# Optimization experiments

Hardware: AMD Instinct MI355X
Metric: run time of the kernel (lower is better)

## Reference

```python
import jax, jax.numpy as jnp
import numpy as np

HEADS = 16
HEAD_DIM = 128


def rotate_half(x):
    x1, x2 = x[..., : x.shape[-1] // 2], x[..., x.shape[-1] // 2 :]
    return jnp.concatenate((-x2, x1), axis=-1)


def setup_inputs() -> dict:
    key = jax.random.key(0)
    ks = jax.random.split(key, 8)
    b, s, h = 2, 2048, 2048
    d = HEAD_DIM
    sc = 1.0 / np.sqrt(h)
    x = jax.random.normal(ks[0], (b, s, h), jnp.float32)
    # real RoPE angles for realism
    inv_freq = 1.0 / (10000.0 ** (jnp.arange(0, d, 2, dtype=jnp.float32) / d))
    t = jnp.arange(s, dtype=jnp.float32)
    freqs = jnp.outer(t, inv_freq)  # [s, d/2]
    emb = jnp.concatenate((freqs, freqs), axis=-1)  # [s, d]
    return {
        "x": x,
        "cos": jnp.cos(emb),
        "sin": jnp.sin(emb),
        "wq": jax.random.normal(ks[1], (h, h), jnp.float32) * sc,
        "bq": jnp.zeros((h,), jnp.float32),
        "wk": jax.random.normal(ks[2], (h, h), jnp.float32) * sc,
        "bk": jnp.zeros((h,), jnp.float32),
        "wv": jax.random.normal(ks[3], (h, h), jnp.float32) * sc,
        "bv": jnp.zeros((h,), jnp.float32),
        "wo": jax.random.normal(ks[4], (h, h), jnp.float32) * sc,
    }


def reference(x, cos, sin, wq, bq, wk, bk, wv, bv, wo):
    b, s, hidden = x.shape
    nh, d = HEADS, HEAD_DIM
    # QKV projections (F.linear: x @ W.T + b)
    def split_heads(t):
        return t.reshape(b, s, nh, d).transpose(0, 2, 1, 3)  # [b,h,s,d]
    q = split_heads(x @ wq.T + bq)
    k = split_heads(x @ wk.T + bk)
    v = split_heads(x @ wv.T + bv)
    # RoPE (cos/sin: [s,d] broadcast over [b,h,s,d])
    q = q * cos + rotate_half(q) * sin
    k = k * cos + rotate_half(k) * sin
    # full (non-causal) attention, materializing [b,h,s,s] scores as original
    scale = 1.0 / jnp.sqrt(jnp.asarray(d, x.dtype))
    scores = jnp.einsum("bhqd,bhkd->bhqk", q, k) * scale
    attn = jax.nn.softmax(scores, axis=-1)
    out = jnp.einsum("bhqk,bhkd->bhqd", attn, v)  # [b,h,s,d]
    out = out.transpose(0, 2, 1, 3).reshape(b, s, hidden)
    # o_proj: no bias
    return out @ wo.T
```

## Files before the change

kernel.cpp:

```cpp
#include <hip/hip_runtime.h>

#define B_  2
#define NH  16
#define S_  2048
#define D_  128
#define HID 2048

typedef _Float16 half_t;
typedef _Float16 f16x8 __attribute__((ext_vector_type(8)));
typedef _Float16 f16x4_t __attribute__((ext_vector_type(4)));
typedef float f32x4 __attribute__((ext_vector_type(4)));

__device__ __forceinline__ void glds16(const half_t* g, half_t* l) {
    __builtin_amdgcn_global_load_lds(
        (const __attribute__((address_space(1))) void*)g,
        (__attribute__((address_space(3))) void*)l, 16, 0, 0);
}
__device__ __forceinline__ float fexp2(float x) { return __builtin_amdgcn_exp2f(x); }

__global__ __launch_bounds__(256) void cvt_all(
    const float* __restrict__ x,  const float* __restrict__ wq, const float* __restrict__ wk,
    const float* __restrict__ wv, const float* __restrict__ wo, half_t* __restrict__ dst)
{
    long i = ((long)blockIdx.x * 256 + threadIdx.x) * 4;
    const float* src; long off;
    if (i < 8388608)       { src = x;  off = i; }
    else if (i < 12582912) { src = wq; off = i - 8388608; }
    else if (i < 16777216) { src = wk; off = i - 12582912; }
    else if (i < 20971520) { src = wv; off = i - 16777216; }
    else                   { src = wo; off = i - 20971520; }
    float4 v = *(const float4*)(src + off);
    f16x4_t h;
    h[0] = (half_t)v.x; h[1] = (half_t)v.y; h[2] = (half_t)v.z; h[3] = (half_t)v.w;
    *(f16x4_t*)(dst + i) = h;
}

__global__ __launch_bounds__(256, 3) void qkv_gemm(
    const half_t* __restrict__ xb,
    const half_t* __restrict__ wqb, const half_t* __restrict__ wkb, const half_t* __restrict__ wvb,
    const float* __restrict__ bq, const float* __restrict__ bk, const float* __restrict__ bv,
    const float* __restrict__ cosp, const float* __restrict__ sinp,
    half_t* __restrict__ qo, half_t* __restrict__ ko, half_t* __restrict__ vto)
{
    __shared__ __align__(16) half_t As[128 * 64];
    __shared__ __align__(16) half_t Bs[128 * 64];
    const int m0 = blockIdx.x * 128;
    const int n0 = blockIdx.y * 128;
    const int z  = blockIdx.z;
    const half_t* wb   = (z == 0) ? wqb : (z == 1) ? wkb : wvb;
    const float*  bias = (z == 0) ? bq  : (z == 1) ? bk  : bv;
    const int tid = threadIdx.x, wave = tid >> 6, lane = tid & 63;
    const int quad = lane >> 4, lrow = lane & 15;
    const int wm = wave >> 1, wn = wave & 1;

    const int sr = wave * 8 + (lane >> 3);
    const int c8 = ((lane & 7) - (lane >> 3)) & 7;
    const half_t* ag = xb + (size_t)(m0 + sr) * HID + c8 * 8;
    const half_t* bg = wb + (size_t)(n0 + sr) * HID + c8 * 8;
    half_t* alb = &As[(wave * 8) * 64];
    half_t* blb = &Bs[(wave * 8) * 64];

    f32x4 acc[4][4] = {};

    for (int k0 = 0; k0 < HID; k0 += 64) {
        __syncthreads();
#pragma unroll
        for (int p = 0; p < 4; ++p) {
            glds16(ag + k0 + (size_t)(p * 32) * HID, alb + p * 32 * 64);
            glds16(bg + k0 + (size_t)(p * 32) * HID, blb + p * 32 * 64);
        }
        __syncthreads();
#pragma unroll
        for (int ks = 0; ks < 2; ++ks) {
            f16x8 af[4], bf[4];
#pragma unroll
            for (int mt = 0; mt < 4; mt++) {
                const int ra = wm * 64 + mt * 16 + lrow;
                const int pa = (ks * 4 + quad + (ra & 7)) & 7;
                af[mt] = *(const f16x8*)&As[ra * 64 + pa * 8];
            }
#pragma unroll
            for (int nt = 0; nt < 4; nt++) {
                const int rb = wn * 16 + nt * 32 + lrow;
                const int pb = (ks * 4 + quad + (rb & 7)) & 7;
                bf[nt] = *(const f16x8*)&Bs[rb * 64 + pb * 8];
            }
#pragma unroll
            for (int mt = 0; mt < 4; mt++)
#pragma unroll
                for (int nt = 0; nt < 4; nt++)
                    acc[mt][nt] = __builtin_amdgcn_mfma_f32_16x16x32_f16(af[mt], bf[nt], acc[mt][nt], 0, 0, 0);
        }
    }

    const int head = blockIdx.y;
    float bs_[4];
#pragma unroll
    for (int nt = 0; nt < 4; nt++) bs_[nt] = bias[n0 + nt * 32 + wn * 16 + lrow];
#pragma unroll
    for (int mt = 0; mt < 4; mt++) {
#pragma unroll
        for (int r = 0; r < 4; r++) {
            const int m  = m0 + wm * 64 + mt * 16 + quad * 4 + r;
            const int bb = m >> 11;
            const int st = m & (S_ - 1);
            float res[4];
#pragma unroll
            for (int nt = 0; nt < 4; nt++) res[nt] = acc[mt][nt][r] + bs_[nt];
            if (z < 2) {
                const float* cr = cosp + st * D_;
                const float* sr2 = sinp + st * D_;
#pragma unroll
                for (int pr = 0; pr < 2; pr++) {
                    const int dlo = pr * 32 + wn * 16 + lrow;
                    float cl = cr[dlo], sl = sr2[dlo], ch = cr[dlo + 64], sh = sr2[dlo + 64];
                    float lo = res[pr], hi = res[pr + 2];
                    res[pr]     = lo * cl - hi * sl;
                    res[pr + 2] = hi * ch + lo * sh;
                }
                half_t* dst = (z == 0 ? qo : ko) + ((size_t)(bb * NH + head) * S_ + st) * D_;
#pragma unroll
                for (int nt = 0; nt < 4; nt++) dst[nt * 32 + wn * 16 + lrow] = (half_t)res[nt];
            } else {
                half_t* dst = vto + (size_t)(bb * NH + head) * D_ * S_ + st;
#pragma unroll
                for (int nt = 0; nt < 4; nt++) dst[(size_t)(nt * 32 + wn * 16 + lrow) * S_] = (half_t)res[nt];
            }
        }
    }
}

#define PLD 72
__global__ __launch_bounds__(256, 2) void attn_kernel(
    const half_t* __restrict__ qb, const half_t* __restrict__ kb,
    const half_t* __restrict__ vtb, half_t* __restrict__ ob)
{
    __shared__ __align__(16) half_t ks[64 * 128];
    __shared__ __align__(16) half_t vs[128 * 64];
    __shared__ __align__(16) half_t ps[4 * 32 * PLD];
    const int head = blockIdx.y, b = blockIdx.z;
    const int bh = b * NH + head;
    const int tid = threadIdx.x, wave = tid >> 6, lane = tid & 63;
    const int quad = lane >> 4, lrow = lane & 15;
    const float SC = 0.08838834764831845f * 1.4426950408889634f;
    const int q0 = blockIdx.x * 128 + wave * 32;

    f16x8 qf[2][4];
#pragma unroll
    for (int mt = 0; mt < 2; mt++) {
        const half_t* qrow = qb + ((size_t)bh * S_ + q0 + mt * 16 + lrow) * D_;
#pragma unroll
        for (int kc = 0; kc < 4; kc++) {
            f16x8 v = *(const f16x8*)(qrow + kc * 32 + quad * 8);
#pragma unroll
            for (int j = 0; j < 8; j++) v[j] = (half_t)((float)v[j] * SC);
            qf[mt][kc] = v;
        }
    }

    const half_t* kbase = kb + (size_t)bh * S_ * D_;
    const half_t* vbase = vtb + (size_t)bh * D_ * S_;
    const int pbase = wave * 32 * PLD;

    f16x8 kreg[4], vreg[4];
#define LOAD_TILE(kt_) do {                                                           \
    _Pragma("unroll")                                                                 \
    for (int i = 0; i < 4; i++) {                                                     \
        const int rk_ = wave * 16 + i * 4 + (lane >> 4);                              \
        const int ck_ = (((lane & 15) - (rk_ & 7)) & 15) * 8;                         \
        kreg[i] = *(const f16x8*)(kbase + (size_t)((kt_) * 64 + rk_) * D_ + ck_);     \
        const int rv_ = wave * 32 + i * 8 + (lane >> 3);                              \
        const int cv_ = (((lane & 7) - (rv_ & 7)) & 7) * 8;                           \
        vreg[i] = *(const f16x8*)(vbase + (size_t)rv_ * S_ + (kt_) * 64 + cv_);       \
    }                                                                                 \
} while (0)
#define WRITE_TILE() do {                                                             \
    _Pragma("unroll")                                                                 \
    for (int i = 0; i < 4; i++) {                                                     \
        *(f16x8*)&ks[(wave * 16 + i * 4) * 128 + lane * 8] = kreg[i];                 \
        *(f16x8*)&vs[(wave * 32 + i * 8) * 64  + lane * 8] = vreg[i];                 \
    }                                                                                 \
} while (0)

    float m_run[2] = {-1e30f, -1e30f}, l_run[2] = {0.f, 0.f};
    f32x4 o[2][8] = {};

    LOAD_TILE(0);
    WRITE_TILE();
    __syncthreads();

    for (int kt = 0; kt < 32; kt++) {
        if (kt + 1 < 32) LOAD_TILE(kt + 1);

        f32x4 st[2][4] = {};
        __builtin_amdgcn_s_setprio(1);
#pragma unroll
        for (int nt = 0; nt < 4; nt++) {
            const int rk2 = nt * 16 + lrow;
#pragma unroll
            for (int kc = 0; kc < 4; kc++) {
                const int pk = (kc * 4 + quad + (rk2 & 7)) & 15;
                f16x8 kf = *(const f16x8*)&ks[rk2 * 128 + pk * 8];
                st[0][nt] = __builtin_amdgcn_mfma_f32_16x16x32_f16(kf, qf[0][kc], st[0][nt], 0, 0, 0);
                st[1][nt] = __builtin_amdgcn_mfma_f32_16x16x32_f16(kf, qf[1][kc], st[1][nt], 0, 0, 0);
            }
        }
        __builtin_amdgcn_s_setprio(0);

        bool upd = false;
        float alpha[2];
#pragma unroll
        for (int mt = 0; mt < 2; mt++) {
            float m01 = fmaxf(fmaxf(st[mt][0][0], st[mt][0][1]), fmaxf(st[mt][0][2], st[mt][0][3]));
            float m11 = fmaxf(fmaxf(st[mt][1][0], st[mt][1][1]), fmaxf(st[mt][1][2], st[mt][1][3]));
            float m21 = fmaxf(fmaxf(st[mt][2][0], st[mt][2][1]), fmaxf(st[mt][2][2], st[mt][2][3]));
            float m31 = fmaxf(fmaxf(st[mt][3][0], st[mt][3][1]), fmaxf(st[mt][3][2], st[mt][3][3]));
            float mx = fmaxf(fmaxf(m01, m11), fmaxf(m21, m31));
            mx = fmaxf(mx, __shfl_xor(mx, 16));
            mx = fmaxf(mx, __shfl_xor(mx, 32));
            const float mnew = fmaxf(m_run[mt], mx);
            alpha[mt] = fexp2(m_run[mt] - mnew);
            upd = upd || (mnew > m_run[mt]);
            m_run[mt] = mnew;
            float rsp[4];
#pragma unroll
            for (int nt = 0; nt < 4; nt++) {
                f16x4_t pk4;
                float r0 = fexp2(st[mt][nt][0] - mnew);
                float r1 = fexp2(st[mt][nt][1] - mnew);
                float r2 = fexp2(st[mt][nt][2] - mnew);
                float r3 = fexp2(st[mt][nt][3] - mnew);
                pk4[0] = (half_t)r0; pk4[1] = (half_t)r1;
                pk4[2] = (half_t)r2; pk4[3] = (half_t)r3;
                rsp[nt] = (r0 + r1) + (r2 + r3);
                *(f16x4_t*)&ps[pbase + (mt * 16 + lrow) * PLD + nt * 16 + quad * 4] = pk4;
            }
            float rs = (rsp[0] + rsp[1]) + (rsp[2] + rsp[3]);
            rs += __shfl_xor(rs, 16);
            rs += __shfl_xor(rs, 32);
            l_run[mt] = l_run[mt] * alpha[mt] + rs;
        }
        if (__any(upd)) {
#pragma unroll
            for (int mt = 0; mt < 2; mt++) {
                float ab[4];
#pragma unroll
                for (int r = 0; r < 4; r++) ab[r] = __shfl(alpha[mt], quad * 4 + r, 16);
#pragma unroll
                for (int dt = 0; dt < 8; dt++)
#pragma unroll
                    for (int r = 0; r < 4; r++) o[mt][dt][r] *= ab[r];
            }
        }

        __builtin_amdgcn_s_setprio(1);
#pragma unroll
        for (int kc2 = 0; kc2 < 2; kc2++) {
            f16x8 pf0 = *(const f16x8*)&ps[pbase + lrow * PLD + kc2 * 32 + quad * 8];
            f16x8 pf1 = *(const f16x8*)&ps[pbase + (16 + lrow) * PLD + kc2 * 32 + quad * 8];
#pragma unroll
            for (int dt = 0; dt < 8; dt++) {
                const int rv2 = dt * 16 + lrow;
                const int pv = (kc2 * 4 + quad + (rv2 & 7)) & 7;
                f16x8 vf = *(const f16x8*)&vs[rv2 * 64 + pv * 8];
                o[0][dt] = __builtin_amdgcn_mfma_f32_16x16x32_f16(pf0, vf, o[0][dt], 0, 0, 0);
                o[1][dt] = __builtin_amdgcn_mfma_f32_16x16x32_f16(pf1, vf, o[1][dt], 0, 0, 0);
            }
        }
        __builtin_amdgcn_s_setprio(0);

        __syncthreads();
        if (kt + 1 < 32) WRITE_TILE();
        __syncthreads();
    }

#pragma unroll
    for (int mt = 0; mt < 2; mt++) {
        const float rl = 1.f / l_run[mt];
        float rb[4];
#pragma unroll
        for (int r = 0; r < 4; r++) rb[r] = __shfl(rl, quad * 4 + r, 16);
#pragma unroll
        for (int dt = 0; dt < 8; dt++) {
            const int d = dt * 16 + lrow;
#pragma unroll
            for (int r = 0; r < 4; r++) {
                const int row = q0 + mt * 16 + quad * 4 + r;
                ob[((size_t)b * S_ + row) * HID + head * D_ + d] = (half_t)(o[mt][dt][r] * rb[r]);
            }
        }
    }
#undef LOAD_TILE
#undef WRITE_TILE
}

__global__ __launch_bounds__(256, 3) void out_gemm(
    const half_t* __restrict__ ab, const half_t* __restrict__ wob, float* __restrict__ out)
{
    __shared__ __align__(16) half_t As[128 * 32];
    __shared__ __align__(16) half_t Bs[128 * 32];
    const int m0 = blockIdx.x * 128;
    const int n0 = blockIdx.y * 128;
    const int tid = threadIdx.x, wave = tid >> 6, lane = tid & 63;
    const int quad = lane >> 4, lrow = lane & 15;
    const int wm = wave >> 1, wn = wave & 1;

    const int r0 = wave * 32 + (lane >> 2);
    const int r1 = r0 + 16;
    const int c0 = (((lane & 3) - (r0 >> 1)) & 3) * 8;
    const int c1 = (((lane & 3) - (r1 >> 1)) & 3) * 8;
    const half_t* ag0 = ab  + (size_t)(m0 + r0) * HID + c0;
    const half_t* ag1 = ab  + (size_t)(m0 + r1) * HID + c1;
    const half_t* bg0 = wob + (size_t)(n0 + r0) * HID + c0;
    const half_t* bg1 = wob + (size_t)(n0 + r1) * HID + c1;
    half_t* al0 = &As[(wave * 32) * 32];
    half_t* al1 = &As[(wave * 32 + 16) * 32];
    half_t* bl0 = &Bs[(wave * 32) * 32];
    half_t* bl1 = &Bs[(wave * 32 + 16) * 32];

    f32x4 acc[4][4] = {};

    for (int k0 = 0; k0 < HID; k0 += 32) {
        __syncthreads();
        glds16(ag0 + k0, al0);
        glds16(ag1 + k0, al1);
        glds16(bg0 + k0, bl0);
        glds16(bg1 + k0, bl1);
        __syncthreads();
        f16x8 af[4], bf[4];
#pragma unroll
        for (int mt = 0; mt < 4; mt++) {
            const int ra = wm * 64 + mt * 16 + lrow;
            const int pa = (quad + (ra >> 1)) & 3;
            af[mt] = *(const f16x8*)&As[ra * 32 + pa * 8];
        }
#pragma unroll
        for (int nt = 0; nt < 4; nt++) {
            const int rb = wn * 16 + nt * 32 + lrow;
            const int pb = (quad + (rb >> 1)) & 3;
            bf[nt] = *(const f16x8*)&Bs[rb * 32 + pb * 8];
        }
#pragma unroll
        for (int mt = 0; mt < 4; mt++)
#pragma unroll
            for (int nt = 0; nt < 4; nt++)
                acc[mt][nt] = __builtin_amdgcn_mfma_f32_16x16x32_f16(af[mt], bf[nt], acc[mt][nt], 0, 0, 0);
    }

#pragma unroll
    for (int mt = 0; mt < 4; mt++)
#pragma unroll
        for (int r = 0; r < 4; r++) {
            const int m = m0 + wm * 64 + mt * 16 + quad * 4 + r;
#pragma unroll
            for (int nt = 0; nt < 4; nt++)
                out[(size_t)m * HID + n0 + nt * 32 + wn * 16 + lrow] = acc[mt][nt][r];
        }
}

extern "C" void kernel_launch(void* const* d_in, const int* in_sizes, int n_in,
                              void* d_out, int out_size, void* d_ws, size_t ws_size,
                              hipStream_t stream)
{
    const float* x    = (const float*)d_in[0];
    const float* cosp = (const float*)d_in[1];
    const float* sinp = (const float*)d_in[2];
    const float* wq   = (const float*)d_in[3];
    const float* bq   = (const float*)d_in[4];
    const float* wk   = (const float*)d_in[5];
    const float* bk   = (const float*)d_in[6];
    const float* wv   = (const float*)d_in[7];
    const float* bv   = (const float*)d_in[8];
    const float* wo   = (const float*)d_in[9];
    float* out = (float*)d_out;

    half_t* w   = (half_t*)d_ws;
    half_t* xb  = w;
    half_t* wqb = xb  + 8388608;
    half_t* wkb = wqb + 4194304;
    half_t* wvb = wkb + 4194304;
    half_t* wob = wvb + 4194304;
    half_t* qo  = wob + 4194304;
    half_t* ko  = qo  + 8388608;
    half_t* vto = ko  + 8388608;
    half_t* ob  = vto + 8388608;

    cvt_all<<<24576, 256, 0, stream>>>(x, wq, wk, wv, wo, xb);
    qkv_gemm<<<dim3(32, 16, 3), 256, 0, stream>>>(xb, wqb, wkb, wvb, bq, bk, bv,
                                                  cosp, sinp, qo, ko, vto);
    attn_kernel<<<dim3(16, 16, 2), 256, 0, stream>>>(qo, ko, vto, ob);
    out_gemm<<<dim3(32, 16), 256, 0, stream>>>(ob, wob, out);
}
```

Baseline: 415.3 us.

## Swizzle block order across XCDs and split K/V LDS writes to drop a barrier

All three GEMM/attention kernels remap the linear block id so that consecutive blocks (which MI355X distributes round-robin across XCDs) land on the same XCD with neighbouring tiles, aiming to improve L2 reuse of shared A/B or K/V data. The attention loop also splits the K and V LDS writes: next K tile is written right after the QK MFMAs (after a barrier), and V after the PV MFMAs, removing one __syncthreads per iteration. The swizzle assumes exact grid sizes (1024 or 512 blocks) and the reordered writes rely on ps/ks/vs hazards being covered by the remaining barriers.

```diff
diff --git a/kernel.cpp b/kernel.cpp
--- a/kernel.cpp
+++ b/kernel.cpp
@@ -44,8 +44,11 @@
 {
     __shared__ __align__(16) half_t As[128 * 64];
     __shared__ __align__(16) half_t Bs[128 * 64];
-    const int m0 = blockIdx.x * 128;
-    const int n0 = blockIdx.y * 128;
+    const int bidl = blockIdx.x + (blockIdx.y << 5);
+    const int swz  = (bidl & 7) * 64 + (bidl >> 3);
+    const int bx = swz & 31, by = swz >> 5;
+    const int m0 = bx * 128;
+    const int n0 = by * 128;
     const int z  = blockIdx.z;
     const half_t* wb   = (z == 0) ? wqb : (z == 1) ? wkb : wvb;
     const float*  bias = (z == 0) ? bq  : (z == 1) ? bk  : bv;
@@ -93,7 +96,7 @@
         }
     }
 
-    const int head = blockIdx.y;
+    const int head = by;
     float bs_[4];
 #pragma unroll
     for (int nt = 0; nt < 4; nt++) bs_[nt] = bias[n0 + nt * 32 + wn * 16 + lrow];
@@ -138,12 +141,14 @@
     __shared__ __align__(16) half_t ks[64 * 128];
     __shared__ __align__(16) half_t vs[128 * 64];
     __shared__ __align__(16) half_t ps[4 * 32 * PLD];
-    const int head = blockIdx.y, b = blockIdx.z;
+    const int bid = blockIdx.x + (blockIdx.y << 4) + (blockIdx.z << 8);
+    const int swz = (bid & 7) * 64 + (bid >> 3);
+    const int qx = swz & 15, head = (swz >> 4) & 15, b = swz >> 8;
     const int bh = b * NH + head;
     const int tid = threadIdx.x, wave = tid >> 6, lane = tid & 63;
     const int quad = lane >> 4, lrow = lane & 15;
     const float SC = 0.08838834764831845f * 1.4426950408889634f;
-    const int q0 = blockIdx.x * 128 + wave * 32;
+    const int q0 = qx * 128 + wave * 32;
 
     f16x8 qf[2][4];
 #pragma unroll
@@ -174,19 +179,23 @@
         vreg[i] = *(const f16x8*)(vbase + (size_t)rv_ * S_ + (kt_) * 64 + cv_);       \
     }                                                                                 \
 } while (0)
-#define WRITE_TILE() do {                                                             \
+#define WRITE_K() do {                                                                \
     _Pragma("unroll")                                                                 \
-    for (int i = 0; i < 4; i++) {                                                     \
+    for (int i = 0; i < 4; i++)                                                       \
         *(f16x8*)&ks[(wave * 16 + i * 4) * 128 + lane * 8] = kreg[i];                 \
+} while (0)
+#define WRITE_V() do {                                                                \
+    _Pragma("unroll")                                                                 \
+    for (int i = 0; i < 4; i++)                                                       \
         *(f16x8*)&vs[(wave * 32 + i * 8) * 64  + lane * 8] = vreg[i];                 \
-    }                                                                                 \
 } while (0)
 
     float m_run[2] = {-1e30f, -1e30f}, l_run[2] = {0.f, 0.f};
     f32x4 o[2][8] = {};
 
     LOAD_TILE(0);
-    WRITE_TILE();
+    WRITE_K();
+    WRITE_V();
     __syncthreads();
 
     for (int kt = 0; kt < 32; kt++) {
@@ -206,6 +215,9 @@
             }
         }
         __builtin_amdgcn_s_setprio(0);
+
+        __syncthreads();
+        if (kt + 1 < 32) WRITE_K();
 
         bool upd = false;
         float alpha[2];
@@ -270,8 +282,7 @@
         __builtin_amdgcn_s_setprio(0);
 
         __syncthreads();
-        if (kt + 1 < 32) WRITE_TILE();
-        __syncthreads();
+        if (kt + 1 < 32) WRITE_V();
     }
 
 #pragma unroll
@@ -291,7 +302,8 @@
         }
     }
 #undef LOAD_TILE
-#undef WRITE_TILE
+#undef WRITE_K
+#undef WRITE_V
 }
 
 __global__ __launch_bounds__(256, 3) void out_gemm(
@@ -299,8 +311,10 @@
 {
     __shared__ __align__(16) half_t As[128 * 32];
     __shared__ __align__(16) half_t Bs[128 * 32];
-    const int m0 = blockIdx.x * 128;
-    const int n0 = blockIdx.y * 128;
+    const int bid = blockIdx.x + (blockIdx.y << 5);
+    const int swz = (bid & 7) * 64 + (bid >> 3);
+    const int m0 = (swz & 31) * 128;
+    const int n0 = (swz >> 5) * 128;
     const int tid = threadIdx.x, wave = tid >> 6, lane = tid & 63;
     const int quad = lane >> 4, lrow = lane & 15;
     const int wm = wave >> 1, wn = wave & 1;
```

Result: no change. 421.7 us (+1.5%).

## Use direct global-to-LDS loads and register shuffles for P in attention

Applied to the files above, without the earlier changes.

The attention kernel now stages K/V tiles with global_load_lds instead of register loads followed by LDS writes. It drops the register prefetch of the next tile, so loads are no longer overlapped with compute. The P matrix is passed between MFMA layouts with cross-lane shuffles instead of an LDS round trip, which frees the ps buffer and lets the kernel raise launch bounds to 3 blocks per SM. The trade is lost load/compute overlap and extra shuffle instructions, in exchange for higher occupancy and less LDS traffic.

```diff
diff --git a/kernel.cpp b/kernel.cpp
--- a/kernel.cpp
+++ b/kernel.cpp
@@ -10,6 +10,8 @@
 typedef _Float16 f16x8 __attribute__((ext_vector_type(8)));
 typedef _Float16 f16x4_t __attribute__((ext_vector_type(4)));
 typedef float f32x4 __attribute__((ext_vector_type(4)));
+typedef unsigned int u32x2 __attribute__((ext_vector_type(2)));
+typedef unsigned int u32x4 __attribute__((ext_vector_type(4)));
 
 __device__ __forceinline__ void glds16(const half_t* g, half_t* l) {
     __builtin_amdgcn_global_load_lds(
@@ -130,14 +132,12 @@
     }
 }
 
-#define PLD 72
-__global__ __launch_bounds__(256, 2) void attn_kernel(
+__global__ __launch_bounds__(256, 3) void attn_kernel(
     const half_t* __restrict__ qb, const half_t* __restrict__ kb,
     const half_t* __restrict__ vtb, half_t* __restrict__ ob)
 {
     __shared__ __align__(16) half_t ks[64 * 128];
     __shared__ __align__(16) half_t vs[128 * 64];
-    __shared__ __align__(16) half_t ps[4 * 32 * PLD];
     const int head = blockIdx.y, b = blockIdx.z;
     const int bh = b * NH + head;
     const int tid = threadIdx.x, wave = tid >> 6, lane = tid & 63;
@@ -160,37 +160,22 @@
 
     const half_t* kbase = kb + (size_t)bh * S_ * D_;
     const half_t* vbase = vtb + (size_t)bh * D_ * S_;
-    const int pbase = wave * 32 * PLD;
-
-    f16x8 kreg[4], vreg[4];
-#define LOAD_TILE(kt_) do {                                                           \
-    _Pragma("unroll")                                                                 \
-    for (int i = 0; i < 4; i++) {                                                     \
-        const int rk_ = wave * 16 + i * 4 + (lane >> 4);                              \
-        const int ck_ = (((lane & 15) - (rk_ & 7)) & 15) * 8;                         \
-        kreg[i] = *(const f16x8*)(kbase + (size_t)((kt_) * 64 + rk_) * D_ + ck_);     \
-        const int rv_ = wave * 32 + i * 8 + (lane >> 3);                              \
-        const int cv_ = (((lane & 7) - (rv_ & 7)) & 7) * 8;                           \
-        vreg[i] = *(const f16x8*)(vbase + (size_t)rv_ * S_ + (kt_) * 64 + cv_);       \
-    }                                                                                 \
-} while (0)
-#define WRITE_TILE() do {                                                             \
-    _Pragma("unroll")                                                                 \
-    for (int i = 0; i < 4; i++) {                                                     \
-        *(f16x8*)&ks[(wave * 16 + i * 4) * 128 + lane * 8] = kreg[i];                 \
-        *(f16x8*)&vs[(wave * 32 + i * 8) * 64  + lane * 8] = vreg[i];                 \
-    }                                                                                 \
-} while (0)
 
     float m_run[2] = {-1e30f, -1e30f}, l_run[2] = {0.f, 0.f};
     f32x4 o[2][8] = {};
 
-    LOAD_TILE(0);
-    WRITE_TILE();
-    __syncthreads();
-
     for (int kt = 0; kt < 32; kt++) {
-        if (kt + 1 < 32) LOAD_TILE(kt + 1);
+        __syncthreads();
+#pragma unroll
+        for (int i = 0; i < 4; i++) {
+            const int rk = wave * 16 + i * 4 + (lane >> 4);
+            const int ck = (((lane & 15) - (rk & 7)) & 15) * 8;
+            glds16(kbase + (size_t)(kt * 64 + rk) * D_ + ck, &ks[(wave * 16 + i * 4) * 128]);
+            const int rv = wave * 32 + i * 8 + (lane >> 3);
+            const int cv = (((lane & 7) - (rv & 7)) & 7) * 8;
+            glds16(vbase + (size_t)rv * S_ + kt * 64 + cv, &vs[(wave * 32 + i * 8) * 64]);
+        }
+        __syncthreads();
 
         f32x4 st[2][4] = {};
         __builtin_amdgcn_s_setprio(1);
@@ -209,6 +194,7 @@
 
         bool upd = false;
         float alpha[2];
+        unsigned int pd[2][4][2];
 #pragma unroll
         for (int mt = 0; mt < 2; mt++) {
             float m01 = fmaxf(fmaxf(st[mt][0][0], st[mt][0][1]), fmaxf(st[mt][0][2], st[mt][0][3]));
@@ -225,15 +211,17 @@
             float rsp[4];
 #pragma unroll
             for (int nt = 0; nt < 4; nt++) {
-                f16x4_t pk4;
                 float r0 = fexp2(st[mt][nt][0] - mnew);
                 float r1 = fexp2(st[mt][nt][1] - mnew);
                 float r2 = fexp2(st[mt][nt][2] - mnew);
                 float r3 = fexp2(st[mt][nt][3] - mnew);
+                f16x4_t pk4;
                 pk4[0] = (half_t)r0; pk4[1] = (half_t)r1;
                 pk4[2] = (half_t)r2; pk4[3] = (half_t)r3;
+                u32x2 dd = __builtin_bit_cast(u32x2, pk4);
+                pd[mt][nt][0] = dd[0];
+                pd[mt][nt][1] = dd[1];
                 rsp[nt] = (r0 + r1) + (r2 + r3);
-                *(f16x4_t*)&ps[pbase + (mt * 16 + lrow) * PLD + nt * 16 + quad * 4] = pk4;
             }
             float rs = (rsp[0] + rsp[1]) + (rsp[2] + rsp[3]);
             rs += __shfl_xor(rs, 16);
@@ -256,22 +244,39 @@
         __builtin_amdgcn_s_setprio(1);
 #pragma unroll
         for (int kc2 = 0; kc2 < 2; kc2++) {
-            f16x8 pf0 = *(const f16x8*)&ps[pbase + lrow * PLD + kc2 * 32 + quad * 8];
-            f16x8 pf1 = *(const f16x8*)&ps[pbase + (16 + lrow) * PLD + kc2 * 32 + quad * 8];
+            f16x8 pf[2];
+#pragma unroll
+            for (int mt = 0; mt < 2; mt++) {
+                unsigned int w0, w1, w2, w3;
+                {
+                    const int src0 = (((quad & 1) * 2 + 0) << 4) | lrow;
+                    const int src1 = (((quad & 1) * 2 + 1) << 4) | lrow;
+                    unsigned int lo0 = __shfl(pd[mt][2 * kc2 + 0][0], src0);
+                    unsigned int hi0 = __shfl(pd[mt][2 * kc2 + 1][0], src0);
+                    unsigned int lo1 = __shfl(pd[mt][2 * kc2 + 0][1], src0);
+                    unsigned int hi1 = __shfl(pd[mt][2 * kc2 + 1][1], src0);
+                    unsigned int lo2 = __shfl(pd[mt][2 * kc2 + 0][0], src1);
+                    unsigned int hi2 = __shfl(pd[mt][2 * kc2 + 1][0], src1);
+                    unsigned int lo3 = __shfl(pd[mt][2 * kc2 + 0][1], src1);
+                    unsigned int hi3 = __shfl(pd[mt][2 * kc2 + 1][1], src1);
+                    w0 = (quad < 2) ? lo0 : hi0;
+                    w1 = (quad < 2) ? lo1 : hi1;
+                    w2 = (quad < 2) ? lo2 : hi2;
+                    w3 = (quad < 2) ? lo3 : hi3;
+                }
+                u32x4 pw = { w0, w1, w2, w3 };
+                pf[mt] = __builtin_bit_cast(f16x8, pw);
+            }
 #pragma unroll
             for (int dt = 0; dt < 8; dt++) {
                 const int rv2 = dt * 16 + lrow;
                 const int pv = (kc2 * 4 + quad + (rv2 & 7)) & 7;
                 f16x8 vf = *(const f16x8*)&vs[rv2 * 64 + pv * 8];
-                o[0][dt] = __builtin_amdgcn_mfma_f32_16x16x32_f16(pf0, vf, o[0][dt], 0, 0, 0);
-                o[1][dt] = __builtin_amdgcn_mfma_f32_16x16x32_f16(pf1, vf, o[1][dt], 0, 0, 0);
+                o[0][dt] = __builtin_amdgcn_mfma_f32_16x16x32_f16(pf[0], vf, o[0][dt], 0, 0, 0);
+                o[1][dt] = __builtin_amdgcn_mfma_f32_16x16x32_f16(pf[1], vf, o[1][dt], 0, 0, 0);
             }
         }
         __builtin_amdgcn_s_setprio(0);
-
-        __syncthreads();
-        if (kt + 1 < 32) WRITE_TILE();
-        __syncthreads();
     }
 
 #pragma unroll
@@ -290,8 +295,6 @@
             }
         }
     }
-#undef LOAD_TILE
-#undef WRITE_TILE
 }
 
 __global__ __launch_bounds__(256, 3) void out_gemm(
```

Measured after the change: 451.8 us. 1.09x slower.
